# Performance work log

Measured on AMD Instinct MI355X. Metric: run time of the kernel, lower is better.

## Reference

```python
import jax, jax.numpy as jnp
import numpy as np
from jax import lax

B, H = 32768, 32  # batch, hidden_dim (hidden_dim=32 fixed by the source module)
T = 128           # num_steps


def setup_inputs() -> dict:
    key = jax.random.key(0)
    ks = jax.random.split(key, 8)
    s = 1.0 / np.sqrt(H)  # torch default uniform(-1/sqrt(H), 1/sqrt(H)) scale
    return {
        "in_data": jax.random.normal(ks[0], (B, H), dtype=jnp.float32),
        "hidden": jax.random.normal(ks[1], (B, H), dtype=jnp.float32),
        "W_ih": jax.random.uniform(ks[2], (3 * H, H), jnp.float32, -s, s),
        "W_hh": jax.random.uniform(ks[3], (3 * H, H), jnp.float32, -s, s),
        "b_ih": jax.random.uniform(ks[4], (3 * H,), jnp.float32, -s, s),
        "b_hh": jax.random.uniform(ks[5], (3 * H,), jnp.float32, -s, s),
        "W_out": jax.random.uniform(ks[6], (1, H), jnp.float32, -s, s),
        "b_out": jax.random.uniform(ks[7], (1,), jnp.float32, -s, s),
        "num_steps": T,
    }


def reference(in_data, hidden, W_ih, W_hh, b_ih, b_hh, W_out, b_out, num_steps):
    # the GRU hidden output is fed back as the next step's input.
    def gru_cell(x, h):
        gi = x @ W_ih.T + b_ih  # [B, 3H]
        gh = h @ W_hh.T + b_hh  # [B, 3H]
        i_r, i_z, i_n = jnp.split(gi, 3, axis=-1)
        h_r, h_z, h_n = jnp.split(gh, 3, axis=-1)
        r = jax.nn.sigmoid(i_r + h_r)
        z = jax.nn.sigmoid(i_z + h_z)
        n = jnp.tanh(i_n + r * h_n)
        return (1.0 - z) * n + z * h

    def step(carry, _):
        x, h = carry
        h_new = gru_cell(x, h)
        y = h_new @ W_out.T + b_out  # [B, 1]
        return (h_new, h_new), y[:, 0]

    _, ys = lax.scan(step, (in_data, hidden), None, length=num_steps)  # ys: [T, B]
    return ys.T  # [B, T], matching torch's stack().squeeze(2).permute(1,0)
```

## Files before the change

kernel.cpp:

```cpp
#include <hip/hip_runtime.h>


typedef __attribute__((ext_vector_type(8)))  short short8;
typedef __attribute__((ext_vector_type(4)))  float f32x4;

struct F3 { short8 h, m, l; };

__device__ __forceinline__ void ldrow8(const float* p, float f[8]) {
    f32x4 a = *(const f32x4*)p;
    f32x4 b = *(const f32x4*)(p + 4);
    f[0]=a[0]; f[1]=a[1]; f[2]=a[2]; f[3]=a[3];
    f[4]=b[0]; f[5]=b[1]; f[6]=b[2]; f[7]=b[3];
}

__device__ __forceinline__ F3 split8(const float f[8]) {
    unsigned H[8], M[8], L[8];
    #pragma unroll
    for (int i = 0; i < 8; ++i) {
        unsigned a = __float_as_uint(f[i]);
        unsigned h = a & 0xffff0000u;
        float    t = f[i] - __uint_as_float(h);
        unsigned m = __float_as_uint(t) & 0xffff0000u;
        float    u = t - __uint_as_float(m);
        unsigned l = __float_as_uint(u) & 0xffff0000u;
        H[i] = h; M[i] = m; L[i] = l;
    }
    union { unsigned u[4]; short8 s; } uh, um, ul;
    #pragma unroll
    for (int p = 0; p < 4; ++p) {
        uh.u[p] = __builtin_amdgcn_perm(H[2*p+1], H[2*p], 0x07060302u);
        um.u[p] = __builtin_amdgcn_perm(M[2*p+1], M[2*p], 0x07060302u);
        ul.u[p] = __builtin_amdgcn_perm(L[2*p+1], L[2*p], 0x07060302u);
    }
    F3 r; r.h = uh.s; r.m = um.s; r.l = ul.s; return r;
}

#define MFMA(a,b,c) __builtin_amdgcn_mfma_f32_16x16x32_bf16((a),(b),(c),0,0,0)

__device__ __forceinline__ f32x4 mm6(const F3& A, const F3& B, f32x4 c) {
    c = MFMA(A.h, B.l, c);
    c = MFMA(A.l, B.h, c);
    c = MFMA(A.m, B.m, c);
    c = MFMA(A.h, B.m, c);
    c = MFMA(A.m, B.h, c);
    c = MFMA(A.h, B.h, c);
    return c;
}

__device__ __forceinline__ float rcp_nr(float x) {
    float r = __builtin_amdgcn_rcpf(x);
    return r * fmaf(-x, r, 2.f);
}
__device__ __forceinline__ float sigm_(float x) {
    x = __builtin_amdgcn_fmed3f(x, -60.f, 60.f);
    return rcp_nr(1.f + __expf(-x));
}
__device__ __forceinline__ float tanh_(float x) {
    x = __builtin_amdgcn_fmed3f(x, -30.f, 30.f);
    return fmaf(-2.f, rcp_nr(__expf(2.f * x) + 1.f), 1.f);
}
__device__ __forceinline__ float comb_(float ar, float az, float an_, float ahn, float hp) {
    float rr = sigm_(ar);
    float zz = sigm_(az);
    float nn = tanh_(fmaf(rr, ahn, an_));
    return fmaf(zz, hp - nn, nn);
}

__global__ __launch_bounds__(256, 2)
void gru_mfma(const float* __restrict__ in_data, const float* __restrict__ hidden,
              const float* __restrict__ W_ih,   const float* __restrict__ W_hh,
              const float* __restrict__ b_ih,   const float* __restrict__ b_hh,
              const float* __restrict__ W_out,  const float* __restrict__ b_out,
              float* __restrict__ out, int B, int T)
{
    __shared__ __align__(16) float hxch[4][16][32];

    const int tid  = threadIdx.x;
    const int lane = tid & 63, wv = tid >> 6;
    const int n    = lane & 15;
    const int g    = lane >> 4;
    const int k0   = g * 8;
    const int c_lo = g * 4;
    const long e   = (long)blockIdx.x * 64 + wv * 16 + n;
    float* hb      = &hxch[wv][0][0];
    const int swz  = (n & 7) * 4;

    f32x4 bC[8];
    #pragma unroll
    for (int tt = 0; tt < 8; ++tt) {
        #pragma unroll
        for (int r = 0; r < 4; ++r) {
            int c = c_lo + r;
            float v;
            if      (tt < 4) { int i = tt * 16 + c;            v = b_ih[i] + b_hh[i]; }
            else if (tt < 6) { int i = 64 + (tt - 4) * 16 + c; v = b_ih[i]; }
            else             { int i = 64 + (tt - 6) * 16 + c; v = b_hh[i]; }
            bC[tt][r] = v;
        }
    }
    float wlo[4], whi[4], hplo[4], hphi[4];
    #pragma unroll
    for (int r = 0; r < 4; ++r) { wlo[r] = W_out[c_lo + r]; whi[r] = W_out[16 + c_lo + r]; }
    {   f32x4 a = *(const f32x4*)(hidden + e * 32 + c_lo);
        f32x4 b = *(const f32x4*)(hidden + e * 32 + 16 + c_lo);
        #pragma unroll
        for (int r = 0; r < 4; ++r) { hplo[r] = a[r]; hphi[r] = b[r]; }
    }
    const float boutv = b_out[0];

    F3 Bx, Bv;
    { float f[8]; ldrow8(in_data + e * 32 + k0, f); Bx = split8(f); }
    { float f[8]; ldrow8(hidden  + e * 32 + k0, f); Bv = split8(f); }

    F3 A[8];
    f32x4 C[8];

    #pragma unroll
    for (int rt = 0; rt < 6; ++rt) {
        float f[8]; ldrow8(W_ih + (rt * 16 + n) * 32 + k0, f);
        A[rt] = split8(f);
    }
    #pragma unroll
    for (int rt = 0; rt < 6; ++rt) C[rt] = mm6(A[rt], Bx, bC[rt]);

    #pragma unroll
    for (int rt = 0; rt < 6; ++rt) {
        float f[8]; ldrow8(W_hh + (rt * 16 + n) * 32 + k0, f);
        A[rt] = split8(f);
    }
    #pragma unroll
    for (int rt = 0; rt < 4; ++rt) C[rt] = mm6(A[rt], Bv, C[rt]);
    C[6] = mm6(A[4], Bv, bC[6]);
    C[7] = mm6(A[5], Bv, bC[7]);

    #pragma unroll
    for (int rt = 0; rt < 8; ++rt) {
        float f[8];
        if (rt < 4) {
            float f2[8];
            ldrow8(W_ih + (rt * 16 + n) * 32 + k0, f);
            ldrow8(W_hh + (rt * 16 + n) * 32 + k0, f2);
            #pragma unroll
            for (int i = 0; i < 8; ++i) f[i] += f2[i];
        } else if (rt < 6) {
            ldrow8(W_ih + (64 + (rt - 4) * 16 + n) * 32 + k0, f);
        } else {
            ldrow8(W_hh + (64 + (rt - 6) * 16 + n) * 32 + k0, f);
        }
        A[rt] = split8(f);
    }

    #pragma unroll 1
    for (int t = 0; t < T; ++t) {
        float hl[4], hh2[4], yp = 0.f;
        #pragma unroll
        for (int r = 0; r < 4; ++r) {
            hl[r]  = comb_(C[0][r], C[2][r], C[4][r], C[6][r], hplo[r]);
            hh2[r] = comb_(C[1][r], C[3][r], C[5][r], C[7][r], hphi[r]);
            yp = fmaf(wlo[r], hl[r], yp);
            yp = fmaf(whi[r], hh2[r], yp);
            hplo[r] = hl[r]; hphi[r] = hh2[r];
        }
        yp += __shfl_xor(yp, 16);
        yp += __shfl_xor(yp, 32);
        if (lane < 16) out[e * T + t] = yp + boutv;
        if (t == T - 1) break;

        {
            f32x4 w0, w1;
            #pragma unroll
            for (int r = 0; r < 4; ++r) { w0[r] = hl[r]; w1[r] = hh2[r]; }
            *(f32x4*)(hb + n * 32 + ((c_lo)      ^ swz)) = w0;
            *(f32x4*)(hb + n * 32 + ((16 + c_lo) ^ swz)) = w1;
            f32x4 r0 = *(const f32x4*)(hb + n * 32 + ((k0)     ^ swz));
            f32x4 r1 = *(const f32x4*)(hb + n * 32 + ((k0 + 4) ^ swz));
            float f[8];
            #pragma unroll
            for (int r = 0; r < 4; ++r) { f[r] = r0[r]; f[4 + r] = r1[r]; }
            Bv = split8(f);
        }

        #pragma unroll
        for (int rt = 0; rt < 8; ++rt) C[rt] = mm6(A[rt], Bv, bC[rt]);
    }
}

extern "C" void kernel_launch(void* const* d_in, const int* in_sizes, int n_in,
                              void* d_out, int out_size, void* d_ws, size_t ws_size,
                              hipStream_t stream) {
    const float* in_data = (const float*)d_in[0];
    const float* hidden  = (const float*)d_in[1];
    const float* W_ih    = (const float*)d_in[2];
    const float* W_hh    = (const float*)d_in[3];
    const float* b_ih    = (const float*)d_in[4];
    const float* b_hh    = (const float*)d_in[5];
    const float* W_out   = (const float*)d_in[6];
    const float* b_out   = (const float*)d_in[7];
    float* out = (float*)d_out;

    const int B = in_sizes[0] / 32;
    const int T = out_size / B;
    const int blocks = B / 64;

    gru_mfma<<<blocks, 256, 0, stream>>>(in_data, hidden, W_ih, W_hh,
                                         b_ih, b_hh, W_out, b_out, out, B, T);
}
```

Measured before the change: 305.0 us.

## Permute weight rows so MFMA output layout matches B-operand layout, removing LDS exchange

Weight rows are loaded in a permuted order (rlo/rhi mapping) so that each lane's MFMA accumulator outputs are exactly the hidden columns it needs for the next step's B operand. This removes the per-step shared-memory write/read round trip, along with its swizzle logic, from the serial recurrence. Biases and W_out are re-indexed to match the new column assignment. The risk is in the permutation: if it does not line up with the MFMA output layout, the results will be wrong.

After: 298.8 us. 2.1% less time.

```diff
diff --git a/kernel.cpp b/kernel.cpp
--- a/kernel.cpp
+++ b/kernel.cpp
@@ -73,60 +73,64 @@
               const float* __restrict__ W_out,  const float* __restrict__ b_out,
               float* __restrict__ out, int B, int T)
 {
-    __shared__ __align__(16) float hxch[4][16][32];
-
     const int tid  = threadIdx.x;
     const int lane = tid & 63, wv = tid >> 6;
     const int n    = lane & 15;
     const int g    = lane >> 4;
     const int k0   = g * 8;
-    const int c_lo = g * 4;
     const long e   = (long)blockIdx.x * 64 + wv * 16 + n;
-    float* hb      = &hxch[wv][0][0];
-    const int swz  = (n & 7) * 4;
+
+    const int rlo = 8 * (n >> 2) + (n & 3);
+    const int rhi = rlo + 4;
 
     f32x4 bC[8];
     #pragma unroll
-    for (int tt = 0; tt < 8; ++tt) {
+    for (int p = 0; p < 2; ++p) {
         #pragma unroll
         for (int r = 0; r < 4; ++r) {
-            int c = c_lo + r;
-            float v;
-            if      (tt < 4) { int i = tt * 16 + c;            v = b_ih[i] + b_hh[i]; }
-            else if (tt < 6) { int i = 64 + (tt - 4) * 16 + c; v = b_ih[i]; }
-            else             { int i = 64 + (tt - 6) * 16 + c; v = b_hh[i]; }
-            bC[tt][r] = v;
+            const int c = 8 * g + 4 * p + r;
+            bC[0 + p][r] = b_ih[c]      + b_hh[c];
+            bC[2 + p][r] = b_ih[32 + c] + b_hh[32 + c];
+            bC[4 + p][r] = b_ih[64 + c];
+            bC[6 + p][r] = b_hh[64 + c];
         }
     }
-    float wlo[4], whi[4], hplo[4], hphi[4];
-    #pragma unroll
-    for (int r = 0; r < 4; ++r) { wlo[r] = W_out[c_lo + r]; whi[r] = W_out[16 + c_lo + r]; }
-    {   f32x4 a = *(const f32x4*)(hidden + e * 32 + c_lo);
-        f32x4 b = *(const f32x4*)(hidden + e * 32 + 16 + c_lo);
-        #pragma unroll
-        for (int r = 0; r < 4; ++r) { hplo[r] = a[r]; hphi[r] = b[r]; }
-    }
+    float wl[4], wh[4];
+    #pragma unroll
+    for (int r = 0; r < 4; ++r) { wl[r] = W_out[8*g + r]; wh[r] = W_out[8*g + 4 + r]; }
     const float boutv = b_out[0];
-
-    F3 Bx, Bv;
-    { float f[8]; ldrow8(in_data + e * 32 + k0, f); Bx = split8(f); }
-    { float f[8]; ldrow8(hidden  + e * 32 + k0, f); Bv = split8(f); }
+    float* const op = out + e * (long)T;
+
+    float hp[8];
+    F3 Bv, Bx;
+    {
+        float f[8]; ldrow8(hidden + e * 32 + k0, f);
+        #pragma unroll
+        for (int i = 0; i < 8; ++i) hp[i] = f[i];
+        Bv = split8(f);
+        float fx[8]; ldrow8(in_data + e * 32 + k0, fx);
+        Bx = split8(fx);
+    }
 
     F3 A[8];
     f32x4 C[8];
 
     #pragma unroll
-    for (int rt = 0; rt < 6; ++rt) {
-        float f[8]; ldrow8(W_ih + (rt * 16 + n) * 32 + k0, f);
-        A[rt] = split8(f);
+    for (int gs = 0; gs < 3; ++gs) {
+        float fl[8], fh[8];
+        ldrow8(W_ih + (gs * 32 + rlo) * 32 + k0, fl);
+        ldrow8(W_ih + (gs * 32 + rhi) * 32 + k0, fh);
+        A[2*gs] = split8(fl); A[2*gs+1] = split8(fh);
     }
     #pragma unroll
     for (int rt = 0; rt < 6; ++rt) C[rt] = mm6(A[rt], Bx, bC[rt]);
 
     #pragma unroll
-    for (int rt = 0; rt < 6; ++rt) {
-        float f[8]; ldrow8(W_hh + (rt * 16 + n) * 32 + k0, f);
-        A[rt] = split8(f);
+    for (int gs = 0; gs < 3; ++gs) {
+        float fl[8], fh[8];
+        ldrow8(W_hh + (gs * 32 + rlo) * 32 + k0, fl);
+        ldrow8(W_hh + (gs * 32 + rhi) * 32 + k0, fh);
+        A[2*gs] = split8(fl); A[2*gs+1] = split8(fh);
     }
     #pragma unroll
     for (int rt = 0; rt < 4; ++rt) C[rt] = mm6(A[rt], Bv, C[rt]);
@@ -134,52 +138,46 @@
     C[7] = mm6(A[5], Bv, bC[7]);
 
     #pragma unroll
-    for (int rt = 0; rt < 8; ++rt) {
-        float f[8];
-        if (rt < 4) {
-            float f2[8];
-            ldrow8(W_ih + (rt * 16 + n) * 32 + k0, f);
-            ldrow8(W_hh + (rt * 16 + n) * 32 + k0, f2);
-            #pragma unroll
-            for (int i = 0; i < 8; ++i) f[i] += f2[i];
-        } else if (rt < 6) {
-            ldrow8(W_ih + (64 + (rt - 4) * 16 + n) * 32 + k0, f);
-        } else {
-            ldrow8(W_hh + (64 + (rt - 6) * 16 + n) * 32 + k0, f);
-        }
-        A[rt] = split8(f);
+    for (int gs = 0; gs < 2; ++gs) {
+        float fl[8], fh[8], g2[8];
+        ldrow8(W_ih + (gs * 32 + rlo) * 32 + k0, fl);
+        ldrow8(W_hh + (gs * 32 + rlo) * 32 + k0, g2);
+        #pragma unroll
+        for (int i = 0; i < 8; ++i) fl[i] += g2[i];
+        ldrow8(W_ih + (gs * 32 + rhi) * 32 + k0, fh);
+        ldrow8(W_hh + (gs * 32 + rhi) * 32 + k0, g2);
+        #pragma unroll
+        for (int i = 0; i < 8; ++i) fh[i] += g2[i];
+        A[2*gs] = split8(fl); A[2*gs+1] = split8(fh);
+    }
+    {
+        float fl[8], fh[8];
+        ldrow8(W_ih + (64 + rlo) * 32 + k0, fl);
+        ldrow8(W_ih + (64 + rhi) * 32 + k0, fh);
+        A[4] = split8(fl); A[5] = split8(fh);
+        ldrow8(W_hh + (64 + rlo) * 32 + k0, fl);
+        ldrow8(W_hh + (64 + rhi) * 32 + k0, fh);
+        A[6] = split8(fl); A[7] = split8(fh);
     }
 
     #pragma unroll 1
     for (int t = 0; t < T; ++t) {
-        float hl[4], hh2[4], yp = 0.f;
+        float h8[8], yp = 0.f;
         #pragma unroll
         for (int r = 0; r < 4; ++r) {
-            hl[r]  = comb_(C[0][r], C[2][r], C[4][r], C[6][r], hplo[r]);
-            hh2[r] = comb_(C[1][r], C[3][r], C[5][r], C[7][r], hphi[r]);
-            yp = fmaf(wlo[r], hl[r], yp);
-            yp = fmaf(whi[r], hh2[r], yp);
-            hplo[r] = hl[r]; hphi[r] = hh2[r];
+            float a  = comb_(C[0][r], C[2][r], C[4][r], C[6][r], hp[r]);
+            float b2 = comb_(C[1][r], C[3][r], C[5][r], C[7][r], hp[4 + r]);
+            yp = fmaf(wl[r], a,  yp);
+            yp = fmaf(wh[r], b2, yp);
+            h8[r] = a; h8[4 + r] = b2;
+            hp[r] = a; hp[4 + r] = b2;
         }
         yp += __shfl_xor(yp, 16);
         yp += __shfl_xor(yp, 32);
-        if (lane < 16) out[e * T + t] = yp + boutv;
+        if (lane < 16) op[t] = yp + boutv;
         if (t == T - 1) break;
 
-        {
-            f32x4 w0, w1;
-            #pragma unroll
-            for (int r = 0; r < 4; ++r) { w0[r] = hl[r]; w1[r] = hh2[r]; }
-            *(f32x4*)(hb + n * 32 + ((c_lo)      ^ swz)) = w0;
-            *(f32x4*)(hb + n * 32 + ((16 + c_lo) ^ swz)) = w1;
-            f32x4 r0 = *(const f32x4*)(hb + n * 32 + ((k0)     ^ swz));
-            f32x4 r1 = *(const f32x4*)(hb + n * 32 + ((k0 + 4) ^ swz));
-            float f[8];
-            #pragma unroll
-            for (int r = 0; r < 4; ++r) { f[r] = r0[r]; f[4 + r] = r1[r]; }
-            Bv = split8(f);
-        }
-
+        Bv = split8(h8);
         #pragma unroll
         for (int rt = 0; rt < 8; ++rt) C[rt] = mm6(A[rt], Bv, bC[rt]);
     }
```
